# Kernel optimization log

Measured on AMD Instinct MI355X. Metric: run time of the kernel, lower is better.

Reference implementation:

```python
import jax, jax.numpy as jnp
import numpy as np

HIDDEN = 1152
N_HEADS = 4
N_KV = 1
HEAD_DIM = 256
EPS = 1e-6
B, S = 4, 2048
ROPE_THETA = 1000000.0


def _rms_norm(x, w):
    # x: [..., D] float32; Gemma-style (1 + w) scale
    xf = x.astype(jnp.float32)
    inv = jax.lax.rsqrt(jnp.mean(xf * xf, axis=-1, keepdims=True) + EPS)
    return (xf * inv * (1.0 + w.astype(jnp.float32))).astype(x.dtype)


def _apply_rope(x, cos, sin):
    # x: [B, H, S, D]; cos/sin: [S, D/2]
    d2 = x.shape[-1] // 2
    x1, x2 = x[..., :d2], x[..., d2:]
    cos = cos[None, None, :, :]
    sin = sin[None, None, :, :]
    xr = x1 * cos - x2 * sin
    xi = x1 * sin + x2 * cos
    return jnp.concatenate([xr, xi], axis=-1).astype(x.dtype)


def setup_inputs() -> dict:
    key = jax.random.key(0)
    k_h, k_qkv, k_qn, k_kn, k_o = jax.random.split(key, 5)
    hidden_states = jax.random.normal(k_h, (B, S, HIDDEN), dtype=jnp.float32)
    # causal additive mask [1,1,S,S]
    neg = jnp.finfo(jnp.float32).min
    causal = jnp.tril(jnp.ones((S, S), dtype=bool))
    attention_mask = jnp.where(causal, 0.0, neg)[None, None, :, :].astype(jnp.float32)
    # RoPE tables (complex freqs_cis split into cos/sin)
    inv_freq = 1.0 / (ROPE_THETA ** (np.arange(0, HEAD_DIM, 2, dtype=np.float32) / HEAD_DIM))
    ang = np.arange(S, dtype=np.float32)[:, None] * inv_freq[None, :]
    freqs_cos = jnp.asarray(np.cos(ang))
    freqs_sin = jnp.asarray(np.sin(ang))
    qkv_out = (N_HEADS + 2 * N_KV) * HEAD_DIM
    scale = HIDDEN ** -0.5
    w_qkv = jax.random.normal(k_qkv, (HIDDEN, qkv_out), dtype=jnp.float32) * scale
    w_o = jax.random.normal(k_o, (N_HEADS * HEAD_DIM, HIDDEN), dtype=jnp.float32) * (N_HEADS * HEAD_DIM) ** -0.5
    q_norm_w = jax.random.normal(k_qn, (HEAD_DIM,), dtype=jnp.float32) * 0.02
    k_norm_w = jax.random.normal(k_kn, (HEAD_DIM,), dtype=jnp.float32) * 0.02
    return {
        "hidden_states": hidden_states,
        "attention_mask": attention_mask,
        "freqs_cos": freqs_cos,
        "freqs_sin": freqs_sin,
        "w_qkv": w_qkv,
        "q_norm_w": q_norm_w,
        "k_norm_w": k_norm_w,
        "w_o": w_o,
    }


def reference(hidden_states, attention_mask, freqs_cos, freqs_sin, w_qkv, q_norm_w, k_norm_w, w_o):
    b, s, _ = hidden_states.shape
    groups = N_HEADS // N_KV
    scaling = HEAD_DIM ** -0.5

    qkv = jnp.einsum("bsh,ho->bso", hidden_states, w_qkv)
    q_end = N_HEADS * HEAD_DIM
    k_end = q_end + N_KV * HEAD_DIM
    q = qkv[:, :, :q_end].reshape(b, s, N_HEADS, HEAD_DIM).transpose(0, 2, 1, 3)
    k = qkv[:, :, q_end:k_end].reshape(b, s, N_KV, HEAD_DIM).transpose(0, 2, 1, 3)
    v = qkv[:, :, k_end:].reshape(b, s, N_KV, HEAD_DIM).transpose(0, 2, 1, 3)

    q = _rms_norm(q, q_norm_w)
    k = _rms_norm(k, k_norm_w)

    q = _apply_rope(q, freqs_cos, freqs_sin)
    k = _apply_rope(k, freqs_cos, freqs_sin)

    if groups > 1:
        k = jnp.repeat(k, groups, axis=1)  # [B, H, S, D]
        v = jnp.repeat(v, groups, axis=1)

    scores = jnp.einsum("bhqd,bhkd->bhqk", q * scaling, k)
    scores = scores + attention_mask.astype(jnp.float32)
    probs = jax.nn.softmax(scores.astype(jnp.float32), axis=-1).astype(q.dtype)

    attn = jnp.einsum("bhqk,bhkd->bhqd", probs, v)
    attn = attn.transpose(0, 2, 1, 3).reshape(b, s, N_HEADS * HEAD_DIM)
    return jnp.einsum("bsf,fh->bsh", attn, w_o)
```

## Files before the change

kernel.cpp:

```cpp
#include <hip/hip_runtime.h>

typedef _Float16 f16;
typedef _Float16 f16x8 __attribute__((ext_vector_type(8)));
typedef _Float16 f16x4 __attribute__((ext_vector_type(4)));
typedef float f32x4 __attribute__((ext_vector_type(4)));

#define NH 4
#define HD 256
#define BB 4
#define SS 2048
#define HID 1152
#define QKV_N 1536
#define ODIM (NH * HD)

#define QKV16_OFF 0L
#define HID16_OFF 25165824L
#define OBUF_OFF 0L
#define OPART_OFF 33554432L
#define QB_OFF 50331648L
#define KB_OFF 67108864L
#define VT_OFF 71303168L
#define WQKVT_OFF 75497472L
#define WOT_OFF 79036416L
#define ML_OFF 81395712L

#define GLL16(gp, lp)                                                      \
  __builtin_amdgcn_global_load_lds(                                       \
      (const __attribute__((address_space(1))) char*)(gp),                \
      (__attribute__((address_space(3))) char*)(lp), 16, 0, 0)

__global__ __launch_bounds__(256) void cvt_f32_to_f16(
    const float* __restrict__ s, f16* __restrict__ d, long n) {
  long i = ((long)blockIdx.x * 256 + threadIdx.x) * 8;
  long stride = (long)gridDim.x * 256 * 8;
  for (; i < n; i += stride) {
    float4 a = *(const float4*)(s + i);
    float4 b = *(const float4*)(s + i + 4);
    f16x8 h = {(f16)a.x, (f16)a.y, (f16)a.z, (f16)a.w,
               (f16)b.x, (f16)b.y, (f16)b.z, (f16)b.w};
    *(f16x8*)(d + i) = h;
  }
}

template <typename ST>
__global__ __launch_bounds__(256) void transpose_cvt(
    const ST* __restrict__ src, long src_ld, long src_bs,
    f16* __restrict__ dst, long dst_ld, long dst_bs) {
  __shared__ float tile[32][33];
  src += (long)blockIdx.z * src_bs;
  dst += (long)blockIdx.z * dst_bs;
  int r0 = blockIdx.y * 32, c0 = blockIdx.x * 32;
  int tc = threadIdx.x & 31, tr = threadIdx.x >> 5;
#pragma unroll
  for (int i = 0; i < 4; ++i)
    tile[tr + i * 8][tc] = (float)src[(long)(r0 + tr + i * 8) * src_ld + c0 + tc];
  __syncthreads();
#pragma unroll
  for (int i = 0; i < 4; ++i)
    dst[(long)(c0 + tr + i * 8) * dst_ld + r0 + tc] = (f16)tile[tc][tr + i * 8];
}

template <typename CT>
__global__ __launch_bounds__(256, 3) void gemm_f16(
    const f16* __restrict__ A, const f16* __restrict__ Bt,
    CT* __restrict__ C, int K, int N) {
  __shared__ f16 As[128][64];
  __shared__ f16 Bs[128][64];
  int tid = threadIdx.x, wave = tid >> 6, lane = tid & 63;
  int l16 = lane & 15, lhi = lane >> 4;
  int wm = (wave >> 1) * 64, wn = (wave & 1) * 64;
  long bm = (long)blockIdx.x * 128, bn = (long)blockIdx.y * 128;
  f32x4 acc[4][4] = {};

  int srow = wave * 32 + (lane >> 3);
  int scol = (lane & 7) * 8;
  const f16* Ag = A + (bm + srow) * (long)K + scol;
  const f16* Bg = Bt + (bn + srow) * (long)K + scol;

  for (int k0 = 0; k0 < K; k0 += 64) {
#pragma unroll
    for (int i = 0; i < 4; ++i)
      GLL16(Ag + k0 + (long)i * 8 * K, &As[wave * 32 + i * 8][0]);
#pragma unroll
    for (int i = 0; i < 4; ++i)
      GLL16(Bg + k0 + (long)i * 8 * K, &Bs[wave * 32 + i * 8][0]);
    __syncthreads();
#pragma unroll
    for (int kb = 0; kb < 2; ++kb) {
      f16x8 af[4], bf[4];
#pragma unroll
      for (int i = 0; i < 4; ++i)
        af[i] = *(const f16x8*)&As[wm + i * 16 + l16][kb * 32 + lhi * 8];
#pragma unroll
      for (int j = 0; j < 4; ++j)
        bf[j] = *(const f16x8*)&Bs[wn + j * 16 + l16][kb * 32 + lhi * 8];
#pragma unroll
      for (int i = 0; i < 4; ++i)
#pragma unroll
        for (int j = 0; j < 4; ++j)
          acc[i][j] =
              __builtin_amdgcn_mfma_f32_16x16x32_f16(bf[j], af[i], acc[i][j], 0, 0, 0);
    }
    __syncthreads();
  }

#pragma unroll
  for (int i = 0; i < 4; ++i) {
    long m = bm + wm + i * 16 + l16;
#pragma unroll
    for (int j = 0; j < 4; ++j) {
      long n = bn + wn + j * 16 + lhi * 4;
      if constexpr (sizeof(CT) == 2) {
        f16x4 h = {(f16)acc[i][j][0], (f16)acc[i][j][1], (f16)acc[i][j][2],
                   (f16)acc[i][j][3]};
        *(f16x4*)&C[m * N + n] = h;
      } else {
        *(f32x4*)&C[m * N + n] = acc[i][j];
      }
    }
  }
}

__device__ __forceinline__ void norm_rope_store(
    const f16* __restrict__ x, const float* __restrict__ w,
    const float* __restrict__ fc, const float* __restrict__ fs,
    f16* __restrict__ dst, float scale, int lane) {
  float x0 = (float)x[lane], x1 = (float)x[lane + 64];
  float x2 = (float)x[lane + 128], x3 = (float)x[lane + 192];
  float ss = x0 * x0 + x1 * x1 + x2 * x2 + x3 * x3;
#pragma unroll
  for (int m = 1; m < 64; m <<= 1) ss += __shfl_xor(ss, m, 64);
  float inv = rsqrtf(ss * (1.0f / 256.0f) + 1e-6f);
  x0 *= inv * (1.0f + w[lane]);
  x1 *= inv * (1.0f + w[lane + 64]);
  x2 *= inv * (1.0f + w[lane + 128]);
  x3 *= inv * (1.0f + w[lane + 192]);
  float c0 = fc[lane], s0 = fs[lane], c1 = fc[lane + 64], s1 = fs[lane + 64];
  dst[lane]       = (f16)((x0 * c0 - x2 * s0) * scale);
  dst[lane + 64]  = (f16)((x1 * c1 - x3 * s1) * scale);
  dst[lane + 128] = (f16)((x0 * s0 + x2 * c0) * scale);
  dst[lane + 192] = (f16)((x1 * s1 + x3 * c1) * scale);
}

__global__ __launch_bounds__(256) void qkv_post(
    const f16* __restrict__ qkv, const float* __restrict__ qnw,
    const float* __restrict__ knw, const float* __restrict__ fcos,
    const float* __restrict__ fsin, f16* __restrict__ Q, f16* __restrict__ Kb) {
  long row = blockIdx.x;
  int b = (int)(row >> 11), s = (int)(row & 2047);
  int wave = threadIdx.x >> 6, lane = threadIdx.x & 63;
  const f16* base = qkv + row * QKV_N;
  const float* fc = fcos + (long)s * 128;
  const float* fs = fsin + (long)s * 128;
  norm_rope_store(base + wave * HD, qnw, fc, fs,
                  Q + ((long)(b * NH + wave) * SS + s) * HD, 0.0625f, lane);
  if (wave == 0)
    norm_rope_store(base + NH * HD, knw, fc, fs, Kb + row * HD, 1.0f, lane);
}

__global__ __launch_bounds__(256, 4) void attn_fwd(
    const f16* __restrict__ Q, const f16* __restrict__ Kb,
    const f16* __restrict__ Vt, f16* __restrict__ O,
    f16* __restrict__ Opart, float2* __restrict__ ml) {
  __shared__ f16 Klds[32 * 256];
  __shared__ f16 Vlds[256 * 32];
  __shared__ f16 Plds[4][16][40];
  int it = blockIdx.x, h = blockIdx.y, b = blockIdx.z;
  int qb, t0, t1, pidx = 0;
  bool split;
  if (it < 16) {
    qb = it; t0 = 0; t1 = 2 * qb + 2; split = false;
  } else {
    int j = it - 16;
    qb = 16 + (j >> 1);
    int s = j & 1, half = qb + 1;
    t0 = s * half; t1 = t0 + half; split = true;
    pidx = (((b * NH + h) << 4) + (qb - 16)) * 2 + s;
  }
  int tid = threadIdx.x, wave = tid >> 6, lane = tid & 63;
  int l16 = lane & 15, lhi = lane >> 4;
  int q0 = qb * 64 + wave * 16;

  const f16* Kg = Kb + (long)b * SS * HD;
  const f16* Vg = Vt + (long)b * HD * SS;

  f16x8 qf[8];
  const f16* Qbase = Q + ((long)(b * NH + h) * SS + q0 + l16) * HD + lhi * 8;
#pragma unroll
  for (int kb = 0; kb < 8; ++kb) qf[kb] = *(const f16x8*)(Qbase + kb * 32);

  f32x4 o[16] = {};
  float m_i = -1e30f, l_i = 0.f;

  int l31 = lane & 31, lh5 = lane >> 5;
  long koff[4];
#pragma unroll
  for (int i = 0; i < 4; ++i) {
    int r = wave * 8 + 2 * i + lh5;
    int csrc = (l31 * 16) ^ (((2 * i + lh5) & 7) << 4);
    koff[i] = (long)r * HD + (csrc >> 1);
  }
  int lh2 = lane >> 2;
  int vcsrc = ((lane & 3) * 16) ^ ((lh2 & 3) << 4);
  long voff[4];
#pragma unroll
  for (int i = 0; i < 4; ++i)
    voff[i] = (long)(wave * 64 + i * 16 + lh2) * SS + (vcsrc >> 1);

  char* kldsb = (char*)Klds + wave * 4096;
  char* vldsb = (char*)Vlds + wave * 4096;

  int kx = (l16 & 7) << 4;
  int vcol = (lhi * 16) ^ ((l16 & 3) << 4);
  const char* krd = (const char*)Klds + l16 * 512;
  const char* vrd = (const char*)Vlds + l16 * 64 + vcol;

  for (int t = t0; t < t1; ++t) {
    long kv0 = (long)t * 32;
    __syncthreads();
#pragma unroll
    for (int i = 0; i < 4; ++i) GLL16(Kg + kv0 * HD + koff[i], kldsb + i * 1024);
#pragma unroll
    for (int i = 0; i < 4; ++i) GLL16(Vg + kv0 + voff[i], vldsb + i * 1024);
    __syncthreads();

    f32x4 sc[2] = {};
    __builtin_amdgcn_s_setprio(1);
#pragma unroll
    for (int kb = 0; kb < 8; ++kb) {
#pragma unroll
      for (int cf = 0; cf < 2; ++cf) {
        f16x8 kf = *(const f16x8*)(krd + cf * 8192 + ((kb * 64 + lhi * 16) ^ kx));
        sc[cf] = __builtin_amdgcn_mfma_f32_16x16x32_f16(kf, qf[kb], sc[cf], 0, 0, 0);
      }
    }
    __builtin_amdgcn_s_setprio(0);

    float p[8];
    float mx = -1e30f;
    int qrow = q0 + l16;
    if (t >= 2 * qb) {
#pragma unroll
      for (int cf = 0; cf < 2; ++cf)
#pragma unroll
        for (int r = 0; r < 4; ++r) {
          int kv = (int)kv0 + cf * 16 + lhi * 4 + r;
          float s = (kv <= qrow) ? sc[cf][r] : -1e30f;
          p[cf * 4 + r] = s;
          mx = fmaxf(mx, s);
        }
    } else {
#pragma unroll
      for (int i = 0; i < 8; ++i) {
        float s = sc[i >> 2][i & 3];
        p[i] = s;
        mx = fmaxf(mx, s);
      }
    }
    mx = fmaxf(mx, __shfl_xor(mx, 16));
    mx = fmaxf(mx, __shfl_xor(mx, 32));
    float mn = fmaxf(m_i, mx);
    float scl = __expf(m_i - mn);
    float rs = 0.f;
#pragma unroll
    for (int i = 0; i < 8; ++i) {
      p[i] = __expf(p[i] - mn);
      rs += p[i];
    }
    rs += __shfl_xor(rs, 16);
    rs += __shfl_xor(rs, 32);
    l_i = l_i * scl + rs;
    m_i = mn;

#pragma unroll
    for (int cf = 0; cf < 2; ++cf) {
      f16x4 hp = {(f16)p[cf * 4], (f16)p[cf * 4 + 1], (f16)p[cf * 4 + 2],
                  (f16)p[cf * 4 + 3]};
      *(f16x4*)&Plds[wave][l16][cf * 16 + lhi * 4] = hp;
    }

    float s0 = __shfl(scl, lhi * 4 + 0);
    float s1 = __shfl(scl, lhi * 4 + 1);
    float s2 = __shfl(scl, lhi * 4 + 2);
    float s3 = __shfl(scl, lhi * 4 + 3);
#pragma unroll
    for (int nf = 0; nf < 16; ++nf) {
      o[nf][0] *= s0;
      o[nf][1] *= s1;
      o[nf][2] *= s2;
      o[nf][3] *= s3;
    }

    f16x8 pa = *(const f16x8*)&Plds[wave][l16][lhi * 8];
    __builtin_amdgcn_s_setprio(1);
#pragma unroll
    for (int nf = 0; nf < 16; ++nf) {
      f16x8 vf = *(const f16x8*)(vrd + nf * 1024);
      o[nf] = __builtin_amdgcn_mfma_f32_16x16x32_f16(pa, vf, o[nf], 0, 0, 0);
    }
    __builtin_amdgcn_s_setprio(0);
  }

  float inv = 1.0f / l_i;
  float i0 = __shfl(inv, lhi * 4 + 0);
  float i1 = __shfl(inv, lhi * 4 + 1);
  float i2 = __shfl(inv, lhi * 4 + 2);
  float i3 = __shfl(inv, lhi * 4 + 3);
  float ir[4] = {i0, i1, i2, i3};
  if (!split) {
#pragma unroll
    for (int r = 0; r < 4; ++r) {
      long srow = q0 + lhi * 4 + r;
      f16* Orow = O + ((long)b * SS + srow) * ODIM + h * HD + l16;
#pragma unroll
      for (int nf = 0; nf < 16; ++nf) Orow[nf * 16] = (f16)(o[nf][r] * ir[r]);
    }
  } else {
#pragma unroll
    for (int r = 0; r < 4; ++r) {
      int rloc = wave * 16 + lhi * 4 + r;
      f16* Prow = Opart + ((long)pidx * 64 + rloc) * HD + l16;
#pragma unroll
      for (int nf = 0; nf < 16; ++nf) Prow[nf * 16] = (f16)(o[nf][r] * ir[r]);
    }
    if (lane < 16) {
      float2 v; v.x = m_i; v.y = l_i;
      ml[(long)pidx * 64 + wave * 16 + lane] = v;
    }
  }
}

__global__ __launch_bounds__(256) void attn_combine(
    const f16* __restrict__ Opart, const float2* __restrict__ ml,
    f16* __restrict__ O) {
  int qx = blockIdx.x, h = blockIdx.y, b = blockIdx.z;
  int qb = 16 + qx;
  int p0 = (((b * NH + h) << 4) + qx) * 2;
  int tid = threadIdx.x;
  int r = tid >> 2, d0 = (tid & 3) * 64;
  float2 a = ml[(long)p0 * 64 + r];
  float2 c = ml[(long)(p0 + 1) * 64 + r];
  float M = fmaxf(a.x, c.x);
  float w0 = a.y * __expf(a.x - M), w1 = c.y * __expf(c.x - M);
  float invL = 1.0f / (w0 + w1);
  w0 *= invL; w1 *= invL;
  const f16* o0 = Opart + ((long)p0 * 64 + r) * HD + d0;
  const f16* o1 = Opart + ((long)(p0 + 1) * 64 + r) * HD + d0;
  f16* Orow = O + ((long)b * SS + qb * 64 + r) * ODIM + h * HD + d0;
#pragma unroll
  for (int i = 0; i < 8; ++i) {
    f16x8 x = *(const f16x8*)(o0 + i * 8);
    f16x8 y = *(const f16x8*)(o1 + i * 8);
    f16x8 z;
#pragma unroll
    for (int j = 0; j < 8; ++j)
      z[j] = (f16)(w0 * (float)x[j] + w1 * (float)y[j]);
    *(f16x8*)(Orow + i * 8) = z;
  }
}

extern "C" void kernel_launch(void* const* d_in, const int* in_sizes, int n_in,
                              void* d_out, int out_size, void* d_ws, size_t ws_size,
                              hipStream_t stream) {
  const float* hidden = (const float*)d_in[0];
  const float* fcos = (const float*)d_in[2];
  const float* fsin = (const float*)d_in[3];
  const float* wqkv = (const float*)d_in[4];
  const float* qnw = (const float*)d_in[5];
  const float* knw = (const float*)d_in[6];
  const float* wo = (const float*)d_in[7];
  float* out = (float*)d_out;

  char* ws = (char*)d_ws;
  f16* qkv16 = (f16*)(ws + QKV16_OFF);
  f16* hid16 = (f16*)(ws + HID16_OFF);
  f16* Obuf = (f16*)(ws + OBUF_OFF);
  f16* Opart = (f16*)(ws + OPART_OFF);
  f16* Qb = (f16*)(ws + QB_OFF);
  f16* Kb = (f16*)(ws + KB_OFF);
  f16* Vt = (f16*)(ws + VT_OFF);
  f16* wqkvt = (f16*)(ws + WQKVT_OFF);
  f16* wot = (f16*)(ws + WOT_OFF);
  float2* ml = (float2*)(ws + ML_OFF);

  cvt_f32_to_f16<<<2048, 256, 0, stream>>>(hidden, hid16, (long)BB * SS * HID);

  transpose_cvt<float><<<dim3(QKV_N / 32, HID / 32, 1), 256, 0, stream>>>(
      wqkv, QKV_N, 0, wqkvt, HID, 0);
  transpose_cvt<float><<<dim3(HID / 32, ODIM / 32, 1), 256, 0, stream>>>(
      wo, HID, 0, wot, ODIM, 0);

  gemm_f16<f16><<<dim3(BB * SS / 128, QKV_N / 128), 256, 0, stream>>>(
      hid16, wqkvt, qkv16, HID, QKV_N);

  qkv_post<<<dim3(BB * SS), 256, 0, stream>>>(qkv16, qnw, knw, fcos, fsin, Qb, Kb);

  transpose_cvt<f16><<<dim3(HD / 32, SS / 32, BB), 256, 0, stream>>>(
      qkv16 + 1280, QKV_N, (long)SS * QKV_N, Vt, SS, (long)HD * SS);

  attn_fwd<<<dim3(48, NH, BB), 256, 0, stream>>>(Qb, Kb, Vt, Obuf, Opart, ml);
  attn_combine<<<dim3(16, NH, BB), 256, 0, stream>>>(Opart, ml, Obuf);

  gemm_f16<float><<<dim3(BB * SS / 128, HID / 128), 256, 0, stream>>>(
      Obuf, wot, out, ODIM, HID);
}
```

Baseline: 253.7 us.

## Fuse fp32 input conversion into QKV GEMM, rebalance attention splits, use register-staged loads

The standalone f32-to-f16 conversion kernel is removed. The QKV GEMM now reads fp32 hidden states directly, converts them in registers and writes them to LDS, which saves one full round trip of the activation tensor through memory. Attention work splitting changes from 16 unsplit plus 2-way splits to 11 unsplit, 2-way and 3-way splits (63 blocks per head), and the combine kernel handles up to 3 partials, to even out per-block work. K/V tile loads switch from global_load_lds to ordinary vector loads plus LDS stores with a new swizzle, which adds register traffic and VGPR pressure.

```diff
diff --git a/kernel.cpp b/kernel.cpp
--- a/kernel.cpp
+++ b/kernel.cpp
@@ -14,33 +14,19 @@
 #define ODIM (NH * HD)
 
 #define QKV16_OFF 0L
-#define HID16_OFF 25165824L
 #define OBUF_OFF 0L
-#define OPART_OFF 33554432L
+#define OPART_OFF 16777216L
+#define ML_OFF 44040192L
 #define QB_OFF 50331648L
 #define KB_OFF 67108864L
 #define VT_OFF 71303168L
 #define WQKVT_OFF 75497472L
 #define WOT_OFF 79036416L
-#define ML_OFF 81395712L
 
 #define GLL16(gp, lp)                                                      \
   __builtin_amdgcn_global_load_lds(                                       \
       (const __attribute__((address_space(1))) char*)(gp),                \
       (__attribute__((address_space(3))) char*)(lp), 16, 0, 0)
-
-__global__ __launch_bounds__(256) void cvt_f32_to_f16(
-    const float* __restrict__ s, f16* __restrict__ d, long n) {
-  long i = ((long)blockIdx.x * 256 + threadIdx.x) * 8;
-  long stride = (long)gridDim.x * 256 * 8;
-  for (; i < n; i += stride) {
-    float4 a = *(const float4*)(s + i);
-    float4 b = *(const float4*)(s + i + 4);
-    f16x8 h = {(f16)a.x, (f16)a.y, (f16)a.z, (f16)a.w,
-               (f16)b.x, (f16)b.y, (f16)b.z, (f16)b.w};
-    *(f16x8*)(d + i) = h;
-  }
-}
 
 template <typename ST>
 __global__ __launch_bounds__(256) void transpose_cvt(
@@ -60,9 +46,9 @@
     dst[(long)(c0 + tr + i * 8) * dst_ld + r0 + tc] = (f16)tile[tc][tr + i * 8];
 }
 
-template <typename CT>
-__global__ __launch_bounds__(256, 3) void gemm_f16(
-    const f16* __restrict__ A, const f16* __restrict__ Bt,
+template <typename AT, typename CT>
+__global__ __launch_bounds__(256, 3) void gemm_x(
+    const AT* __restrict__ A, const f16* __restrict__ Bt,
     CT* __restrict__ C, int K, int N) {
   __shared__ f16 As[128][64];
   __shared__ f16 Bs[128][64];
@@ -72,15 +58,37 @@
   long bm = (long)blockIdx.x * 128, bn = (long)blockIdx.y * 128;
   f32x4 acc[4][4] = {};
 
-  int srow = wave * 32 + (lane >> 3);
-  int scol = (lane & 7) * 8;
-  const f16* Ag = A + (bm + srow) * (long)K + scol;
+  int srow = wave * 32 + (lane >> 3), scol = (lane & 7) * 8;
   const f16* Bg = Bt + (bn + srow) * (long)K + scol;
+  const f16* Agh = nullptr;
+  const float* Agf = nullptr;
+  int ar = tid >> 2, ac = (tid & 3) * 16;
+  if constexpr (sizeof(AT) == 2)
+    Agh = (const f16*)A + (bm + srow) * (long)K + scol;
+  else
+    Agf = (const float*)A + (bm + ar) * (long)K + ac;
 
   for (int k0 = 0; k0 < K; k0 += 64) {
-#pragma unroll
-    for (int i = 0; i < 4; ++i)
-      GLL16(Ag + k0 + (long)i * 8 * K, &As[wave * 32 + i * 8][0]);
+    if constexpr (sizeof(AT) == 2) {
+#pragma unroll
+      for (int i = 0; i < 4; ++i)
+        GLL16(Agh + k0 + (long)i * 8 * K, &As[wave * 32 + i * 8][0]);
+    } else {
+#pragma unroll
+      for (int g = 0; g < 2; ++g) {
+        const float* src = Agf + k0 + (long)g * 64 * K;
+        float4 v0 = *(const float4*)(src + 0);
+        float4 v1 = *(const float4*)(src + 4);
+        float4 v2 = *(const float4*)(src + 8);
+        float4 v3 = *(const float4*)(src + 12);
+        f16x8 h0 = {(f16)v0.x, (f16)v0.y, (f16)v0.z, (f16)v0.w,
+                    (f16)v1.x, (f16)v1.y, (f16)v1.z, (f16)v1.w};
+        f16x8 h1 = {(f16)v2.x, (f16)v2.y, (f16)v2.z, (f16)v2.w,
+                    (f16)v3.x, (f16)v3.y, (f16)v3.z, (f16)v3.w};
+        *(f16x8*)&As[ar + 64 * g][ac] = h0;
+        *(f16x8*)&As[ar + 64 * g][ac + 8] = h1;
+      }
+    }
 #pragma unroll
     for (int i = 0; i < 4; ++i)
       GLL16(Bg + k0 + (long)i * 8 * K, &Bs[wave * 32 + i * 8][0]);
@@ -166,16 +174,23 @@
   __shared__ f16 Vlds[256 * 32];
   __shared__ f16 Plds[4][16][40];
   int it = blockIdx.x, h = blockIdx.y, b = blockIdx.z;
-  int qb, t0, t1, pidx = 0;
+  int qb, t0, t1, slot = 0;
   bool split;
-  if (it < 16) {
+  if (it < 11) {
     qb = it; t0 = 0; t1 = 2 * qb + 2; split = false;
   } else {
-    int j = it - 16;
-    qb = 16 + (j >> 1);
-    int s = j & 1, half = qb + 1;
-    t0 = s * half; t1 = t0 + half; split = true;
-    pidx = (((b * NH + h) << 4) + (qb - 16)) * 2 + s;
+    int j = it - 11, c, nch, lbase;
+    if (j < 22) {
+      qb = 11 + (j >> 1); c = j & 1; nch = 2; lbase = (qb - 11) * 2;
+    } else {
+      int jj = j - 22, q3 = jj / 3;
+      qb = 22 + q3; c = jj - q3 * 3; nch = 3; lbase = 22 + q3 * 3;
+    }
+    int tiles = 2 * qb + 2;
+    t0 = tiles * c / nch;
+    t1 = tiles * (c + 1) / nch;
+    split = true;
+    slot = (b * NH + h) * 52 + lbase + c;
   }
   int tid = threadIdx.x, wave = tid >> 6, lane = tid & 63;
   int l16 = lane & 15, lhi = lane >> 4;
@@ -192,36 +207,29 @@
   f32x4 o[16] = {};
   float m_i = -1e30f, l_i = 0.f;
 
-  int l31 = lane & 31, lh5 = lane >> 5;
-  long koff[4];
-#pragma unroll
-  for (int i = 0; i < 4; ++i) {
-    int r = wave * 8 + 2 * i + lh5;
-    int csrc = (l31 * 16) ^ (((2 * i + lh5) & 7) << 4);
-    koff[i] = (long)r * HD + (csrc >> 1);
-  }
-  int lh2 = lane >> 2;
-  int vcsrc = ((lane & 3) * 16) ^ ((lh2 & 3) << 4);
-  long voff[4];
-#pragma unroll
-  for (int i = 0; i < 4; ++i)
-    voff[i] = (long)(wave * 64 + i * 16 + lh2) * SS + (vcsrc >> 1);
-
-  char* kldsb = (char*)Klds + wave * 4096;
-  char* vldsb = (char*)Vlds + wave * 4096;
-
-  int kx = (l16 & 7) << 4;
-  int vcol = (lhi * 16) ^ ((l16 & 3) << 4);
-  const char* krd = (const char*)Klds + l16 * 512;
-  const char* vrd = (const char*)Vlds + l16 * 64 + vcol;
+  int kr = tid >> 5, kc16 = (tid & 31) * 16;
+  int rv = tid >> 2, vc16 = (tid & 3) * 16;
+  char* kls = (char*)Klds;
+  char* vls = (char*)Vlds;
+  int kwsw = kc16 ^ (kr << 4);
+  int vwsw = vc16 ^ ((rv & 3) << 4);
+  const char* krd = kls + l16 * 512;
+  int kswz = (l16 & 7) << 4;
+  const char* vrd = vls + l16 * 64 + ((lhi * 16) ^ ((l16 & 3) << 4));
 
   for (int t = t0; t < t1; ++t) {
     long kv0 = (long)t * 32;
     __syncthreads();
 #pragma unroll
-    for (int i = 0; i < 4; ++i) GLL16(Kg + kv0 * HD + koff[i], kldsb + i * 1024);
-#pragma unroll
-    for (int i = 0; i < 4; ++i) GLL16(Vg + kv0 + voff[i], vldsb + i * 1024);
+    for (int i = 0; i < 4; ++i) {
+      uint4 kval = *(const uint4*)((const char*)(Kg + (kv0 + kr + 8 * i) * HD) + kc16);
+      *(uint4*)(kls + (kr + 8 * i) * 512 + kwsw) = kval;
+    }
+#pragma unroll
+    for (int i = 0; i < 4; ++i) {
+      uint4 vval = *(const uint4*)((const char*)(Vg + (long)(rv + 64 * i) * SS + kv0) + vc16);
+      *(uint4*)(vls + (rv + 64 * i) * 64 + vwsw) = vval;
+    }
     __syncthreads();
 
     f32x4 sc[2] = {};
@@ -230,7 +238,7 @@
     for (int kb = 0; kb < 8; ++kb) {
 #pragma unroll
       for (int cf = 0; cf < 2; ++cf) {
-        f16x8 kf = *(const f16x8*)(krd + cf * 8192 + ((kb * 64 + lhi * 16) ^ kx));
+        f16x8 kf = *(const f16x8*)(krd + cf * 8192 + ((kb * 64 + lhi * 16) ^ kswz));
         sc[cf] = __builtin_amdgcn_mfma_f32_16x16x32_f16(kf, qf[kb], sc[cf], 0, 0, 0);
       }
     }
@@ -319,13 +327,13 @@
 #pragma unroll
     for (int r = 0; r < 4; ++r) {
       int rloc = wave * 16 + lhi * 4 + r;
-      f16* Prow = Opart + ((long)pidx * 64 + rloc) * HD + l16;
+      f16* Prow = Opart + ((long)slot * 64 + rloc) * HD + l16;
 #pragma unroll
       for (int nf = 0; nf < 16; ++nf) Prow[nf * 16] = (f16)(o[nf][r] * ir[r]);
     }
     if (lane < 16) {
       float2 v; v.x = m_i; v.y = l_i;
-      ml[(long)pidx * 64 + wave * 16 + lane] = v;
+      ml[(long)slot * 64 + wave * 16 + lane] = v;
     }
   }
 }
@@ -333,28 +341,44 @@
 __global__ __launch_bounds__(256) void attn_combine(
     const f16* __restrict__ Opart, const float2* __restrict__ ml,
     f16* __restrict__ O) {
-  int qx = blockIdx.x, h = blockIdx.y, b = blockIdx.z;
-  int qb = 16 + qx;
-  int p0 = (((b * NH + h) << 4) + qx) * 2;
+  int x = blockIdx.x, h = blockIdx.y, b = blockIdx.z;
+  int qb = 11 + x;
+  int nch = (qb < 22) ? 2 : 3;
+  int lbase = (qb < 22) ? (qb - 11) * 2 : 22 + (qb - 22) * 3;
+  long slot0 = (long)(b * NH + h) * 52 + lbase;
   int tid = threadIdx.x;
   int r = tid >> 2, d0 = (tid & 3) * 64;
-  float2 a = ml[(long)p0 * 64 + r];
-  float2 c = ml[(long)(p0 + 1) * 64 + r];
-  float M = fmaxf(a.x, c.x);
-  float w0 = a.y * __expf(a.x - M), w1 = c.y * __expf(c.x - M);
-  float invL = 1.0f / (w0 + w1);
-  w0 *= invL; w1 *= invL;
-  const f16* o0 = Opart + ((long)p0 * 64 + r) * HD + d0;
-  const f16* o1 = Opart + ((long)(p0 + 1) * 64 + r) * HD + d0;
+  float m[3], l[3], w[3];
+  float M = -1e30f;
+#pragma unroll
+  for (int c = 0; c < 3; ++c)
+    if (c < nch) {
+      float2 v = ml[(slot0 + c) * 64 + r];
+      m[c] = v.x; l[c] = v.y;
+      M = fmaxf(M, v.x);
+    }
+  float sum = 0.f;
+#pragma unroll
+  for (int c = 0; c < 3; ++c)
+    if (c < nch) { w[c] = l[c] * __expf(m[c] - M); sum += w[c]; }
+  float inv = 1.0f / sum;
+#pragma unroll
+  for (int c = 0; c < 3; ++c)
+    if (c < nch) w[c] *= inv;
   f16* Orow = O + ((long)b * SS + qb * 64 + r) * ODIM + h * HD + d0;
 #pragma unroll
   for (int i = 0; i < 8; ++i) {
-    f16x8 x = *(const f16x8*)(o0 + i * 8);
-    f16x8 y = *(const f16x8*)(o1 + i * 8);
+    float acc[8] = {};
+#pragma unroll
+    for (int c = 0; c < 3; ++c)
+      if (c < nch) {
+        f16x8 xv = *(const f16x8*)(Opart + ((slot0 + c) * 64 + r) * HD + d0 + i * 8);
+#pragma unroll
+        for (int j = 0; j < 8; ++j) acc[j] += w[c] * (float)xv[j];
+      }
     f16x8 z;
 #pragma unroll
-    for (int j = 0; j < 8; ++j)
-      z[j] = (f16)(w0 * (float)x[j] + w1 * (float)y[j]);
+    for (int j = 0; j < 8; ++j) z[j] = (f16)acc[j];
     *(f16x8*)(Orow + i * 8) = z;
   }
 }
@@ -373,34 +397,31 @@
 
   char* ws = (char*)d_ws;
   f16* qkv16 = (f16*)(ws + QKV16_OFF);
-  f16* hid16 = (f16*)(ws + HID16_OFF);
   f16* Obuf = (f16*)(ws + OBUF_OFF);
   f16* Opart = (f16*)(ws + OPART_OFF);
+  float2* ml = (float2*)(ws + ML_OFF);
   f16* Qb = (f16*)(ws + QB_OFF);
   f16* Kb = (f16*)(ws + KB_OFF);
   f16* Vt = (f16*)(ws + VT_OFF);
   f16* wqkvt = (f16*)(ws + WQKVT_OFF);
   f16* wot = (f16*)(ws + WOT_OFF);
-  float2* ml = (float2*)(ws + ML_OFF);
-
-  cvt_f32_to_f16<<<2048, 256, 0, stream>>>(hidden, hid16, (long)BB * SS * HID);
 
   transpose_cvt<float><<<dim3(QKV_N / 32, HID / 32, 1), 256, 0, stream>>>(
       wqkv, QKV_N, 0, wqkvt, HID, 0);
   transpose_cvt<float><<<dim3(HID / 32, ODIM / 32, 1), 256, 0, stream>>>(
       wo, HID, 0, wot, ODIM, 0);
 
-  gemm_f16<f16><<<dim3(BB * SS / 128, QKV_N / 128), 256, 0, stream>>>(
-      hid16, wqkvt, qkv16, HID, QKV_N);
+  gemm_x<float, f16><<<dim3(BB * SS / 128, QKV_N / 128), 256, 0, stream>>>(
+      hidden, wqkvt, qkv16, HID, QKV_N);
 
   qkv_post<<<dim3(BB * SS), 256, 0, stream>>>(qkv16, qnw, knw, fcos, fsin, Qb, Kb);
 
   transpose_cvt<f16><<<dim3(HD / 32, SS / 32, BB), 256, 0, stream>>>(
       qkv16 + 1280, QKV_N, (long)SS * QKV_N, Vt, SS, (long)HD * SS);
 
-  attn_fwd<<<dim3(48, NH, BB), 256, 0, stream>>>(Qb, Kb, Vt, Obuf, Opart, ml);
-  attn_combine<<<dim3(16, NH, BB), 256, 0, stream>>>(Opart, ml, Obuf);
-
-  gemm_f16<float><<<dim3(BB * SS / 128, HID / 128), 256, 0, stream>>>(
+  attn_fwd<<<dim3(63, NH, BB), 256, 0, stream>>>(Qb, Kb, Vt, Obuf, Opart, ml);
+  attn_combine<<<dim3(21, NH, BB), 256, 0, stream>>>(Opart, ml, Obuf);
+
+  gemm_x<f16, float><<<dim3(BB * SS / 128, HID / 128), 256, 0, stream>>>(
       Obuf, wot, out, ODIM, HID);
 }
```

Result: slower. 279.5 us (+10.2%).
